# Optimization experiments

Hardware: AMD Instinct MI355X
Metric: run time of the kernel (lower is better)

Reference implementation:

```python
import jax, jax.numpy as jnp
import numpy as np

K, R, KAPPA = 4, 16384, 32
NX, NF, DOUT = 3, 13, 64


def setup_inputs() -> dict:
    key = jax.random.key(0)
    ks = jax.random.split(key, 6)
    X = jax.random.normal(ks[0], (K, R, NX), dtype=jnp.float32)
    F = jax.random.normal(ks[1], (K, R, NF), dtype=jnp.float32)
    N = jax.random.randint(ks[2], (K, R, KAPPA), 0, R, dtype=jnp.int32)
    H = jax.random.normal(ks[3], (DOUT, NX + NF), dtype=jnp.float32) * 0.1
    gamma = jax.random.normal(ks[4], (DOUT, DOUT), dtype=jnp.float32) * 0.1
    gamma_bias = jax.random.normal(ks[5], (DOUT,), dtype=jnp.float32) * 0.1
    return {"X": X, "F": F, "N": N, "H": H, "gamma": gamma, "gamma_bias": gamma_bias}


def reference(X, F, N, H, gamma, gamma_bias):
    # P = [X | F] : [K, R, n]
    P = jnp.concatenate([X, F], axis=2)
    # batched gather (tf.gather batch_dims=1): P_groups[k, r, i, :] = P[k, N[k, r, i], :]
    P_groups = jax.vmap(lambda p, n: p[n])(P, N)  # [K, R, kappa, n]
    # SharedMLP: P_groups @ H^T, then relu (H_activation)
    PHT = jax.nn.relu(jnp.einsum('krin,dn->krid', P_groups, H))
    # component-wise max over neighbors
    PHT_max = jnp.max(PHT, axis=2)  # [K, R, Dout]
    # Dense: (P* Gamma) + bias, then relu (gamma_activation)
    Y = jnp.einsum('krd,de->kre', PHT_max, gamma) + gamma_bias
    return jax.nn.relu(Y)
```

## Files before the change

### kernel.cpp

```cpp
#include <hip/hip_runtime.h>
#include <hip/hip_fp16.h>
#include <math.h>

#define KR 65536
#define KAPPA 32

typedef __attribute__((ext_vector_type(8))) _Float16 f16x8;
typedef __attribute__((ext_vector_type(4))) float f32x4;

__global__ __launch_bounds__(256) void q_kernel(
    const float* __restrict__ X, const float* __restrict__ F,
    const float* __restrict__ H, _Float16* __restrict__ Q) {
  __shared__ float Pl[64 * 16];
  const int t = threadIdx.x;
  const int base = blockIdx.x * 64;

  if (t < 192) Pl[(t / 3) * 16 + (t % 3)] = X[(size_t)base * 3 + t];
  for (int j = t; j < 832; j += 256)
    Pl[(j / 13) * 16 + 3 + (j % 13)] = F[(size_t)base * 13 + j];

  const int lane = t & 63, wave = t >> 6;
  const float4 h0 = *(const float4*)(H + lane * 16 + 0);
  const float4 h1 = *(const float4*)(H + lane * 16 + 4);
  const float4 h2 = *(const float4*)(H + lane * 16 + 8);
  const float4 h3 = *(const float4*)(H + lane * 16 + 12);
  __syncthreads();

  #pragma unroll 4
  for (int p = 0; p < 16; ++p) {
    const int lp = wave * 16 + p;
    const float4* pp = (const float4*)(Pl + lp * 16);
    const float4 p0 = pp[0], p1 = pp[1], p2 = pp[2], p3 = pp[3];
    float q = p0.x * h0.x + p0.y * h0.y + p0.z * h0.z + p0.w * h0.w
            + p1.x * h1.x + p1.y * h1.y + p1.z * h1.z + p1.w * h1.w
            + p2.x * h2.x + p2.y * h2.y + p2.z * h2.z + p2.w * h2.w
            + p3.x * h3.x + p3.y * h3.y + p3.z * h3.z + p3.w * h3.w;
    Q[(size_t)(base + lp) * 64 + lane] = (_Float16)q;
  }
}

__global__ __launch_bounds__(256) void gather_gemm_kernel(
    const _Float16* __restrict__ Q, const int* __restrict__ N,
    const float* __restrict__ gamma, const float* __restrict__ gbias,
    float* __restrict__ Y) {
  __shared__ _Float16 Gt[64 * 72];
  __shared__ _Float16 Ml[32 * 72];
  __shared__ float Bl[64];

  const int t = threadIdx.x;
  #pragma unroll
  for (int ii = 0; ii < 4; ++ii) {
    const int i = t + ii * 256;
    const float4 gv = ((const float4*)gamma)[i];
    const int d = i >> 4, e0 = (i & 15) * 4;
    Gt[(e0 + 0) * 72 + d] = (_Float16)gv.x;
    Gt[(e0 + 1) * 72 + d] = (_Float16)gv.y;
    Gt[(e0 + 2) * 72 + d] = (_Float16)gv.z;
    Gt[(e0 + 3) * 72 + d] = (_Float16)gv.w;
  }
  if (t < 64) Bl[t] = gbias[t];

  const int b = blockIdx.x;
  const int xcd = b & 7, bi = b >> 3;
  const int k = xcd >> 1, halfsel = xcd & 1;
  const int base = k * 16384 + (halfsel * 256 + bi) * 32;

  const int lane = t & 63, wave = t >> 6;
  const int grp = lane >> 3, member = lane & 7;
  const _Float16* Qk = Q + ((size_t)k << 20);

  const int mypt = base + wave * 8 + grp;
  const int4* nbase = (const int4*)(N + (size_t)mypt * KAPPA);

  int4 c0 = nbase[0], c1 = nbase[1], c2 = nbase[2], c3 = nbase[3];
  int4 c4 = nbase[4], c5 = nbase[5], c6 = nbase[6], c7 = nbase[7];

  f16x8 m = {0, 0, 0, 0, 0, 0, 0, 0};
  const _Float16* qb = Qk + member * 8;
  #define GSTEP(c)                                                            \
    {                                                                         \
      const f16x8 v0 = *(const f16x8*)(qb + (size_t)(c).x * 64);              \
      const f16x8 v1 = *(const f16x8*)(qb + (size_t)(c).y * 64);              \
      const f16x8 v2 = *(const f16x8*)(qb + (size_t)(c).z * 64);              \
      const f16x8 v3 = *(const f16x8*)(qb + (size_t)(c).w * 64);              \
      const f16x8 t01 = __builtin_elementwise_max(v0, v1);                    \
      const f16x8 t23 = __builtin_elementwise_max(v2, v3);                    \
      m = __builtin_elementwise_max(m, __builtin_elementwise_max(t01, t23));  \
    }
  GSTEP(c0) GSTEP(c1) GSTEP(c2) GSTEP(c3)
  GSTEP(c4) GSTEP(c5) GSTEP(c6) GSTEP(c7)
  #undef GSTEP

  *(f16x8*)(Ml + (wave * 8 + grp) * 72 + member * 8) = m;
  __syncthreads();

  const int ln15 = lane & 15, quad = lane >> 4;
  const int rt = wave & 1, ct = wave >> 1;
  f32x4 acc[2] = {{0.f, 0.f, 0.f, 0.f}, {0.f, 0.f, 0.f, 0.f}};
  #pragma unroll
  for (int ks = 0; ks < 2; ++ks) {
    const f16x8 af = *(const f16x8*)(Ml + (rt * 16 + ln15) * 72 + ks * 32 + quad * 8);
    #pragma unroll
    for (int nt = 0; nt < 2; ++nt) {
      const f16x8 bf = *(const f16x8*)(Gt + (ct * 32 + nt * 16 + ln15) * 72 + ks * 32 + quad * 8);
      acc[nt] = __builtin_amdgcn_mfma_f32_16x16x32_f16(af, bf, acc[nt], 0, 0, 0);
    }
  }

  #pragma unroll
  for (int nt = 0; nt < 2; ++nt) {
    const float bv = Bl[ct * 32 + nt * 16 + ln15];
    #pragma unroll
    for (int r = 0; r < 4; ++r) {
      const float y = fmaxf(acc[nt][r] + bv, 0.0f);
      Y[(size_t)(base + rt * 16 + quad * 4 + r) * 64 + ct * 32 + nt * 16 + ln15] = y;
    }
  }
}

extern "C" void kernel_launch(void* const* d_in, const int* in_sizes, int n_in,
                              void* d_out, int out_size, void* d_ws, size_t ws_size,
                              hipStream_t stream) {
  const float* X  = (const float*)d_in[0];
  const float* F  = (const float*)d_in[1];
  const int*   N  = (const int*)d_in[2];
  const float* H  = (const float*)d_in[3];
  const float* G  = (const float*)d_in[4];
  const float* Gb = (const float*)d_in[5];
  float* Y = (float*)d_out;
  _Float16* Q = (_Float16*)d_ws;

  q_kernel<<<1024, 256, 0, stream>>>(X, F, H, Q);
  gather_gemm_kernel<<<2048, 256, 0, stream>>>(Q, N, G, Gb, Y);
}
```

Baseline: 99.64 us.

## Gather packed fp16 inputs and recompute H projection with MFMA per neighbor

Replaces the precomputed 64-wide projected table Q with a packed 16-wide fp16 copy of [X|F]. The fused kernel now gathers the 16-element neighbor rows and applies H to them with 32x32x16 MFMAs before taking the max. This cuts gathered bytes per neighbor by a factor of four and shrinks the workspace, at the cost of redundant matrix math per neighbor and more register pressure. It also uses nontemporal loads for N and nontemporal stores for Y, and drops the XCD-aware block remapping.

```diff
diff --git a/kernel.cpp b/kernel.cpp
--- a/kernel.cpp
+++ b/kernel.cpp
@@ -3,46 +3,47 @@
 #include <math.h>
 
 #define KR 65536
+#define RS 16384
 #define KAPPA 32
 
 typedef __attribute__((ext_vector_type(8))) _Float16 f16x8;
 typedef __attribute__((ext_vector_type(4))) float f32x4;
+typedef __attribute__((ext_vector_type(16))) float f32x16;
 
-__global__ __launch_bounds__(256) void q_kernel(
+__global__ __launch_bounds__(256) void pack_kernel(
     const float* __restrict__ X, const float* __restrict__ F,
-    const float* __restrict__ H, _Float16* __restrict__ Q) {
-  __shared__ float Pl[64 * 16];
-  const int t = threadIdx.x;
-  const int base = blockIdx.x * 64;
+    const float* __restrict__ H, _Float16* __restrict__ Pp,
+    _Float16* __restrict__ Hp) {
+  const int p = blockIdx.x * 256 + threadIdx.x;
+  const size_t qx = (size_t)p * 3, qf = (size_t)p * 13;
+  f16x8 lo, hi;
+  lo[0] = (_Float16)X[qx + 0];
+  lo[1] = (_Float16)X[qx + 1];
+  lo[2] = (_Float16)X[qx + 2];
+  #pragma unroll
+  for (int j = 0; j < 5; ++j) lo[3 + j] = (_Float16)F[qf + j];
+  #pragma unroll
+  for (int j = 0; j < 8; ++j) hi[j] = (_Float16)F[qf + 5 + j];
+  *(f16x8*)(Pp + (size_t)p * 16 + 0) = lo;
+  *(f16x8*)(Pp + (size_t)p * 16 + 8) = hi;
 
-  if (t < 192) Pl[(t / 3) * 16 + (t % 3)] = X[(size_t)base * 3 + t];
-  for (int j = t; j < 832; j += 256)
-    Pl[(j / 13) * 16 + 3 + (j % 13)] = F[(size_t)base * 13 + j];
-
-  const int lane = t & 63, wave = t >> 6;
-  const float4 h0 = *(const float4*)(H + lane * 16 + 0);
-  const float4 h1 = *(const float4*)(H + lane * 16 + 4);
-  const float4 h2 = *(const float4*)(H + lane * 16 + 8);
-  const float4 h3 = *(const float4*)(H + lane * 16 + 12);
-  __syncthreads();
-
-  #pragma unroll 4
-  for (int p = 0; p < 16; ++p) {
-    const int lp = wave * 16 + p;
-    const float4* pp = (const float4*)(Pl + lp * 16);
-    const float4 p0 = pp[0], p1 = pp[1], p2 = pp[2], p3 = pp[3];
-    float q = p0.x * h0.x + p0.y * h0.y + p0.z * h0.z + p0.w * h0.w
-            + p1.x * h1.x + p1.y * h1.y + p1.z * h1.z + p1.w * h1.w
-            + p2.x * h2.x + p2.y * h2.y + p2.z * h2.z + p2.w * h2.w
-            + p3.x * h3.x + p3.y * h3.y + p3.z * h3.z + p3.w * h3.w;
-    Q[(size_t)(base + lp) * 64 + lane] = (_Float16)q;
+  if (blockIdx.x == 0 && threadIdx.x < 64) {
+    const int d = threadIdx.x;
+    f16x8 a, b;
+    #pragma unroll
+    for (int j = 0; j < 8; ++j) {
+      a[j] = (_Float16)H[d * 16 + j];
+      b[j] = (_Float16)H[d * 16 + 8 + j];
+    }
+    *(f16x8*)(Hp + d * 16 + 0) = a;
+    *(f16x8*)(Hp + d * 16 + 8) = b;
   }
 }
 
-__global__ __launch_bounds__(256) void gather_gemm_kernel(
-    const _Float16* __restrict__ Q, const int* __restrict__ N,
-    const float* __restrict__ gamma, const float* __restrict__ gbias,
-    float* __restrict__ Y) {
+__global__ __launch_bounds__(256) void fused_kernel(
+    const _Float16* __restrict__ Pp, const _Float16* __restrict__ Hp,
+    const int* __restrict__ N, const float* __restrict__ gamma,
+    const float* __restrict__ gbias, float* __restrict__ Y) {
   __shared__ _Float16 Gt[64 * 72];
   __shared__ _Float16 Ml[32 * 72];
   __shared__ float Bl[64];
@@ -60,38 +61,46 @@
   }
   if (t < 64) Bl[t] = gbias[t];
 
-  const int b = blockIdx.x;
-  const int xcd = b & 7, bi = b >> 3;
-  const int k = xcd >> 1, halfsel = xcd & 1;
-  const int base = k * 16384 + (halfsel * 256 + bi) * 32;
+  const int lane = t & 63, wave = t >> 6;
+  const int l31 = lane & 31, hsel = lane >> 5;
 
-  const int lane = t & 63, wave = t >> 6;
-  const int grp = lane >> 3, member = lane & 7;
-  const _Float16* Qk = Q + ((size_t)k << 20);
+  const int base = blockIdx.x * 32;
+  const int k = blockIdx.x >> 9;
+  const _Float16* Pk = Pp + ((size_t)k * RS) * 16;
 
-  const int mypt = base + wave * 8 + grp;
-  const int4* nbase = (const int4*)(N + (size_t)mypt * KAPPA);
+  const f16x8 hb0 = *(const f16x8*)(Hp + (0  + l31) * 16 + hsel * 8);
+  const f16x8 hb1 = *(const f16x8*)(Hp + (32 + l31) * 16 + hsel * 8);
 
-  int4 c0 = nbase[0], c1 = nbase[1], c2 = nbase[2], c3 = nbase[3];
-  int4 c4 = nbase[4], c5 = nbase[5], c6 = nbase[6], c7 = nbase[7];
+  const int p0 = base + wave * 8;
+  int idx[8];
+  #pragma unroll
+  for (int j = 0; j < 8; ++j)
+    idx[j] = __builtin_nontemporal_load(N + (size_t)(p0 + j) * KAPPA + l31);
 
-  f16x8 m = {0, 0, 0, 0, 0, 0, 0, 0};
-  const _Float16* qb = Qk + member * 8;
-  #define GSTEP(c)                                                            \
-    {                                                                         \
-      const f16x8 v0 = *(const f16x8*)(qb + (size_t)(c).x * 64);              \
-      const f16x8 v1 = *(const f16x8*)(qb + (size_t)(c).y * 64);              \
-      const f16x8 v2 = *(const f16x8*)(qb + (size_t)(c).z * 64);              \
-      const f16x8 v3 = *(const f16x8*)(qb + (size_t)(c).w * 64);              \
-      const f16x8 t01 = __builtin_elementwise_max(v0, v1);                    \
-      const f16x8 t23 = __builtin_elementwise_max(v2, v3);                    \
-      m = __builtin_elementwise_max(m, __builtin_elementwise_max(t01, t23));  \
-    }
-  GSTEP(c0) GSTEP(c1) GSTEP(c2) GSTEP(c3)
-  GSTEP(c4) GSTEP(c5) GSTEP(c6) GSTEP(c7)
-  #undef GSTEP
-
-  *(f16x8*)(Ml + (wave * 8 + grp) * 72 + member * 8) = m;
+  const f32x16 z = {0.f, 0.f, 0.f, 0.f, 0.f, 0.f, 0.f, 0.f,
+                    0.f, 0.f, 0.f, 0.f, 0.f, 0.f, 0.f, 0.f};
+  #pragma unroll
+  for (int j = 0; j < 8; ++j) {
+    const f16x8 a = *(const f16x8*)(Pk + (size_t)idx[j] * 16 + hsel * 8);
+    const f32x16 c0 = __builtin_amdgcn_mfma_f32_32x32x16_f16(a, hb0, z, 0, 0, 0);
+    const f32x16 c1 = __builtin_amdgcn_mfma_f32_32x32x16_f16(a, hb1, z, 0, 0, 0);
+    float m0 = fmaxf(
+        fmaxf(fmaxf(fmaxf(c0[0], c0[1]), fmaxf(c0[2], c0[3])),
+              fmaxf(fmaxf(c0[4], c0[5]), fmaxf(c0[6], c0[7]))),
+        fmaxf(fmaxf(fmaxf(c0[8], c0[9]), fmaxf(c0[10], c0[11])),
+              fmaxf(fmaxf(c0[12], c0[13]), fmaxf(c0[14], c0[15]))));
+    float m1 = fmaxf(
+        fmaxf(fmaxf(fmaxf(c1[0], c1[1]), fmaxf(c1[2], c1[3])),
+              fmaxf(fmaxf(c1[4], c1[5]), fmaxf(c1[6], c1[7]))),
+        fmaxf(fmaxf(fmaxf(c1[8], c1[9]), fmaxf(c1[10], c1[11])),
+              fmaxf(fmaxf(c1[12], c1[13]), fmaxf(c1[14], c1[15]))));
+    m0 = fmaxf(m0, 0.0f);
+    m1 = fmaxf(m1, 0.0f);
+    m0 = fmaxf(m0, __shfl_xor(m0, 32, 64));
+    m1 = fmaxf(m1, __shfl_xor(m1, 32, 64));
+    const float ms = hsel ? m1 : m0;
+    Ml[(wave * 8 + j) * 72 + lane] = (_Float16)ms;
+  }
   __syncthreads();
 
   const int ln15 = lane & 15, quad = lane >> 4;
@@ -113,7 +122,8 @@
     #pragma unroll
     for (int r = 0; r < 4; ++r) {
       const float y = fmaxf(acc[nt][r] + bv, 0.0f);
-      Y[(size_t)(base + rt * 16 + quad * 4 + r) * 64 + ct * 32 + nt * 16 + ln15] = y;
+      __builtin_nontemporal_store(
+          y, Y + (size_t)(base + rt * 16 + quad * 4 + r) * 64 + ct * 32 + nt * 16 + ln15);
     }
   }
 }
@@ -128,8 +138,9 @@
   const float* G  = (const float*)d_in[4];
   const float* Gb = (const float*)d_in[5];
   float* Y = (float*)d_out;
-  _Float16* Q = (_Float16*)d_ws;
+  _Float16* Pp = (_Float16*)d_ws;
+  _Float16* Hp = Pp + (size_t)KR * 16;
 
-  q_kernel<<<1024, 256, 0, stream>>>(X, F, H, Q);
-  gather_gemm_kernel<<<2048, 256, 0, stream>>>(Q, N, G, Gb, Y);
+  pack_kernel<<<256, 256, 0, stream>>>(X, F, H, Pp, Hp);
+  fused_kernel<<<2048, 256, 0, stream>>>(Pp, Hp, N, G, Gb, Y);
 }
```

Measured after the change: 95.51 us. 1.04x faster.
